# Performance work log

Measured on AMD Instinct MI355X. Metric: run time of the kernel, lower is better.

Reference implementation:

```python
import jax, jax.numpy as jnp
import numpy as np

N_HEAD, D_MODEL, D_K, D_V = 16, 1024, 64, 64
B, L = 8, 1024
LN_EPS = 1e-5
NEG_INF = -1e9


def setup_inputs() -> dict:
    key = jax.random.key(0)
    ks = jax.random.split(key, 12)
    s = 0.02
    return {
        "q": jax.random.normal(ks[0], (B, L, D_MODEL), jnp.float32),
        "k": jax.random.normal(ks[1], (B, L, D_MODEL), jnp.float32),
        "v": jax.random.normal(ks[2], (B, L, D_MODEL), jnp.float32),
        "mask": jnp.zeros((B, L, L), dtype=bool),
        "wq": jax.random.normal(ks[3], (D_MODEL, N_HEAD * D_K), jnp.float32) * s,
        "bq": jnp.zeros((N_HEAD * D_K,), jnp.float32),
        "wk": jax.random.normal(ks[4], (D_MODEL, N_HEAD * D_K), jnp.float32) * s,
        "bk": jnp.zeros((N_HEAD * D_K,), jnp.float32),
        "wv": jax.random.normal(ks[5], (D_MODEL, N_HEAD * D_V), jnp.float32) * s,
        "bv": jnp.zeros((N_HEAD * D_V,), jnp.float32),
        "wo": jax.random.normal(ks[6], (N_HEAD * D_V, D_MODEL), jnp.float32) * s,
        "bo": jnp.zeros((D_MODEL,), jnp.float32),
        "gamma": jnp.ones((D_MODEL,), jnp.float32),
        "beta": jnp.zeros((D_MODEL,), jnp.float32),
    }


def reference(q, k, v, mask, wq, bq, wk, bk, wv, bv, wo, bo, gamma, beta):
    b, lq, _ = q.shape
    lk = k.shape[1]
    residual = q
    # separate Q/K/V projections, split heads: [b, len, h, d]
    qh = (q @ wq + bq).reshape(b, lq, N_HEAD, D_K)
    kh = (k @ wk + bk).reshape(b, lk, N_HEAD, D_K)
    vh = (v @ wv + bv).reshape(b, lk, N_HEAD, D_V)
    # scaled dot-product attention (temperature = sqrt(d_k))
    scores = jnp.einsum("bqhd,bkhd->bhqk", qh, kh) / jnp.sqrt(jnp.float32(D_K))
    scores = jnp.where(mask[:, None, :, :], NEG_INF, scores)
    attn = jax.nn.softmax(scores, axis=-1)  # [b, h, lq, lk]
    ctx = jnp.einsum("bhqk,bkhd->bqhd", attn, vh).reshape(b, lq, N_HEAD * D_V)
    # out-proj (dropout is identity in eval) + residual + LayerNorm
    out = ctx @ wo + bo + residual
    mu = out.mean(-1, keepdims=True)
    var = out.var(-1, keepdims=True)
    out = (out - mu) * jax.lax.rsqrt(var + LN_EPS) * gamma + beta
    # match original attn layout: [n_head*b, lq, lk]
    attn_flat = attn.transpose(1, 0, 2, 3).reshape(N_HEAD * b, lq, lk)
    return out, attn_flat
```

## Files before the change

### kernel.cpp

```cpp
#include <hip/hip_runtime.h>
#include <stdint.h>

static constexpr int BATCH  = 8;
static constexpr int SEQ    = 1024;
static constexpr int DMODEL = 1024;
static constexpr int NHEAD  = 16;

typedef __attribute__((ext_vector_type(8))) short sh8;
typedef __attribute__((ext_vector_type(4))) float fl4;

__device__ __forceinline__ uint16_t f2bf(float f) {
    union { float f; uint32_t u; } a; a.f = f;
    uint32_t r = a.u + 0x7FFFu + ((a.u >> 16) & 1u);
    return (uint16_t)(r >> 16);
}

__device__ __forceinline__ float b2f(uint16_t u) {
    union { uint32_t u; float f; } a; a.u = ((uint32_t)u) << 16; return a.f;
}

__device__ __forceinline__ uint32_t cvtpk(float lo, float hi) {
    uint32_t r;
    asm("v_cvt_pk_bf16_f32 %0, %1, %2" : "=v"(r) : "v"(lo), "v"(hi));
    return r;
}

__device__ __forceinline__ sh8 pack_bf8(fl4 x0, fl4 x1) {
    union { uint32_t w[4]; sh8 v; } pk;
    pk.w[0] = cvtpk(x0[0], x0[1]); pk.w[1] = cvtpk(x0[2], x0[3]);
    pk.w[2] = cvtpk(x1[0], x1[1]); pk.w[3] = cvtpk(x1[2], x1[3]);
    return pk.v;
}

__device__ __forceinline__ fl4 mfma16(sh8 a, sh8 b, fl4 c) {
    return __builtin_amdgcn_mfma_f32_16x16x32_bf16(a, b, c, 0, 0, 0);
}

__device__ __forceinline__ void gload16(const void* g, void* l) {
    __builtin_amdgcn_global_load_lds(
        (const __attribute__((address_space(1))) void*)g,
        (__attribute__((address_space(3))) void*)l, 16, 0, 0);
}

__global__ __launch_bounds__(256) void prep_kernel(const float* __restrict__ wq, const float* __restrict__ wk,
                                                   const float* __restrict__ wv, const float* __restrict__ wo,
                                                   uint16_t* __restrict__ tq, uint16_t* __restrict__ tk,
                                                   uint16_t* __restrict__ tv, uint16_t* __restrict__ to) {
    __shared__ uint16_t T[64][72];
    const int z = blockIdx.z;
    const int tid = threadIdx.x;
    const float* w = (z == 0) ? wq : (z == 1) ? wk : (z == 2) ? wv : wo;
    uint16_t* wT = (z == 0) ? tq : (z == 1) ? tk : (z == 2) ? tv : to;
    const float ws = (z == 0) ? 0.125f : 1.f;
    const int n0 = blockIdx.x * 64, k0 = blockIdx.y * 64;
    #pragma unroll
    for (int it = 0; it < 4; ++it) {
        int g = it * 256 + tid;
        int r = g >> 4, c = (g & 15) * 4;
        fl4 x = *(const fl4*)(w + (size_t)(k0 + r) * DMODEL + n0 + c);
        T[r][c + 0] = f2bf(x[0] * ws); T[r][c + 1] = f2bf(x[1] * ws);
        T[r][c + 2] = f2bf(x[2] * ws); T[r][c + 3] = f2bf(x[3] * ws);
    }
    __syncthreads();
    #pragma unroll
    for (int it = 0; it < 4; ++it) {
        int g = it * 256 + tid;
        int r = g >> 4, c = (g & 15) * 4;
        ushort4 o;
        o.x = T[c + 0][r]; o.y = T[c + 1][r]; o.z = T[c + 2][r]; o.w = T[c + 3][r];
        *(ushort4*)(wT + (size_t)(n0 + r) * DMODEL + k0 + c) = o;
    }
}

__global__ __launch_bounds__(256)
void gemm_proj(const float* __restrict__ q, const float* __restrict__ k, const float* __restrict__ v,
               const uint16_t* __restrict__ B0, const uint16_t* __restrict__ B1, const uint16_t* __restrict__ B2,
               const float* __restrict__ b0, const float* __restrict__ b1, const float* __restrict__ b2,
               uint16_t* __restrict__ qh, uint16_t* __restrict__ kh, uint16_t* __restrict__ vT) {
    __shared__ uint16_t lds[128 * 128];
    uint16_t* Alds = lds;
    uint16_t* Blds = lds + 128 * 64;
    const int z = blockIdx.z;
    const float* Af    = (z == 0) ? q : (z == 1) ? k : v;
    const uint16_t* Bt = (z == 0) ? B0 : (z == 1) ? B1 : B2;
    const float* bias  = (z == 0) ? b0 : (z == 1) ? b1 : b2;
    const float bs     = (z == 0) ? 0.125f : 1.f;
    const int m0 = blockIdx.x * 128, n0 = blockIdx.y * 128;
    const int tid = threadIdx.x, lane = tid & 63, wid = tid >> 6;
    const int wr = (wid >> 1) * 64, wc = (wid & 1) * 64;
    const int fr = lane & 15, fk = (lane >> 4) * 8, frow4 = (lane >> 4) * 4;

    fl4 acc[4][4];
    #pragma unroll
    for (int i = 0; i < 4; ++i)
        #pragma unroll
        for (int j = 0; j < 4; ++j) acc[i][j] = (fl4){0.f, 0.f, 0.f, 0.f};

    fl4 pa0[4], pa1[4];
    #pragma unroll
    for (int it = 0; it < 4; ++it) {
        const int g = it * 256 + tid;
        const int r = g >> 3, c = (g & 7) << 3;
        const float* p = Af + (size_t)(m0 + r) * DMODEL + c;
        pa0[it] = *(const fl4*)p; pa1[it] = *(const fl4*)(p + 4);
    }

    for (int kt = 0; kt < 16; ++kt) {
        const int kb = kt * 64;
        #pragma unroll
        for (int it = 0; it < 4; ++it) {
            const int g = it * 256 + tid;
            const int r = g >> 3, c = (g & 7) << 3;
            *(sh8*)&Alds[r * 64 + c] = pack_bf8(pa0[it], pa1[it]);
            const int lofs = __builtin_amdgcn_readfirstlane((it * 256 + wid * 64) * 16);
            gload16(Bt + (size_t)(n0 + r) * DMODEL + kb + c, (char*)Blds + lofs);
        }
        __syncthreads();
        if (kt < 15) {
            #pragma unroll
            for (int it = 0; it < 4; ++it) {
                const int g = it * 256 + tid;
                const int r = g >> 3, c = (g & 7) << 3;
                const float* p = Af + (size_t)(m0 + r) * DMODEL + kb + 64 + c;
                pa0[it] = *(const fl4*)p; pa1[it] = *(const fl4*)(p + 4);
            }
        }
        #pragma unroll
        for (int ks = 0; ks < 2; ++ks) {
            sh8 a[4], bb[4];
            #pragma unroll
            for (int mi = 0; mi < 4; ++mi) a[mi] = *(const sh8*)&Alds[(wr + mi * 16 + fr) * 64 + ks * 32 + fk];
            #pragma unroll
            for (int ni = 0; ni < 4; ++ni) bb[ni] = *(const sh8*)&Blds[(wc + ni * 16 + fr) * 64 + ks * 32 + fk];
            #pragma unroll
            for (int mi = 0; mi < 4; ++mi)
                #pragma unroll
                for (int ni = 0; ni < 4; ++ni) acc[mi][ni] = mfma16(a[mi], bb[ni], acc[mi][ni]);
        }
        __syncthreads();
    }

    if (z < 2) {
        #pragma unroll
        for (int mi = 0; mi < 4; ++mi) {
            #pragma unroll
            for (int ni = 0; ni < 4; ++ni) {
                const int col = wc + ni * 16 + fr;
                const float bv = bias[n0 + col] * bs;
                #pragma unroll
                for (int i = 0; i < 4; ++i) {
                    const int row = wr + mi * 16 + frow4 + i;
                    lds[row * 128 + ((((col >> 3) ^ (row & 7)) << 3) | (col & 7))] = f2bf(acc[mi][ni][i] + bv);
                }
            }
        }
        __syncthreads();
        uint16_t* Cv = (z == 0) ? qh : kh;
        #pragma unroll
        for (int it = 0; it < 8; ++it) {
            const int ch = it * 256 + tid;
            const int row = ch >> 4, cc = ch & 15;
            sh8 vv = *(sh8*)&lds[row * 128 + ((cc ^ (row & 7)) << 3)];
            *(sh8*)(Cv + (size_t)(m0 + row) * DMODEL + n0 + cc * 8) = vv;
        }
    } else {
        #pragma unroll
        for (int mi = 0; mi < 4; ++mi) {
            #pragma unroll
            for (int ni = 0; ni < 4; ++ni) {
                const int col = wc + ni * 16 + fr;
                const float bv = bias[n0 + col];
                #pragma unroll
                for (int i = 0; i < 4; ++i) {
                    const int row = wr + mi * 16 + frow4 + i;
                    lds[col * 128 + ((((row >> 3) ^ (col & 7)) << 3) | (row & 7))] = f2bf(acc[mi][ni][i] + bv);
                }
            }
        }
        __syncthreads();
        const int b = m0 >> 10, l0 = m0 & 1023;
        #pragma unroll
        for (int it = 0; it < 8; ++it) {
            const int ch = it * 256 + tid;
            const int col = ch >> 4, rc = ch & 15;
            sh8 vv = *(sh8*)&lds[col * 128 + ((rc ^ (col & 7)) << 3)];
            *(sh8*)(vT + (size_t)(b * 1024 + n0 + col) * SEQ + l0 + rc * 8) = vv;
        }
    }
}

__global__ __launch_bounds__(256)
void gemm_out(const uint16_t* __restrict__ Ab, const uint16_t* __restrict__ Bt,
              const float* __restrict__ bias, const float* __restrict__ resid,
              float* __restrict__ Cv) {
    __shared__ uint16_t lds[128 * 128];
    uint16_t* Alds = lds;
    uint16_t* Blds = lds + 128 * 64;
    const int m0 = blockIdx.x * 128, n0 = blockIdx.y * 128;
    const int tid = threadIdx.x, lane = tid & 63, wid = tid >> 6;
    const int wr = (wid >> 1) * 64, wc = (wid & 1) * 64;
    const int fr = lane & 15, fk = (lane >> 4) * 8, frow4 = (lane >> 4) * 4;

    fl4 acc[4][4];
    #pragma unroll
    for (int i = 0; i < 4; ++i)
        #pragma unroll
        for (int j = 0; j < 4; ++j) acc[i][j] = (fl4){0.f, 0.f, 0.f, 0.f};

    for (int kt = 0; kt < 16; ++kt) {
        const int kb = kt * 64;
        #pragma unroll
        for (int it = 0; it < 4; ++it) {
            const int g = it * 256 + tid;
            const int r = g >> 3, c = (g & 7) << 3;
            const int lofs = __builtin_amdgcn_readfirstlane((it * 256 + wid * 64) * 16);
            gload16(Ab + (size_t)(m0 + r) * DMODEL + kb + c, (char*)Alds + lofs);
            gload16(Bt + (size_t)(n0 + r) * DMODEL + kb + c, (char*)Blds + lofs);
        }
        __syncthreads();
        #pragma unroll
        for (int ks = 0; ks < 2; ++ks) {
            sh8 a[4], bb[4];
            #pragma unroll
            for (int mi = 0; mi < 4; ++mi) a[mi] = *(const sh8*)&Alds[(wr + mi * 16 + fr) * 64 + ks * 32 + fk];
            #pragma unroll
            for (int ni = 0; ni < 4; ++ni) bb[ni] = *(const sh8*)&Blds[(wc + ni * 16 + fr) * 64 + ks * 32 + fk];
            #pragma unroll
            for (int mi = 0; mi < 4; ++mi)
                #pragma unroll
                for (int ni = 0; ni < 4; ++ni) acc[mi][ni] = mfma16(a[mi], bb[ni], acc[mi][ni]);
        }
        __syncthreads();
    }

    float* flds = (float*)lds;
    #pragma unroll
    for (int h2 = 0; h2 < 2; ++h2) {
        if (h2) __syncthreads();
        if (wc == h2 * 64) {
            #pragma unroll
            for (int ni = 0; ni < 4; ++ni) {
                const int col = wc + ni * 16 + fr;
                const int ch = col - h2 * 64;
                const float bv = bias[n0 + col];
                #pragma unroll
                for (int mi = 0; mi < 4; ++mi) {
                    #pragma unroll
                    for (int i = 0; i < 4; ++i) {
                        const int row = wr + mi * 16 + frow4 + i;
                        float val = acc[mi][ni][i] + bv;
                        val += resid[(size_t)(m0 + row) * DMODEL + n0 + col];
                        flds[row * 64 + ((((ch >> 2) ^ (row & 7)) << 2) | (ch & 3))] = val;
                    }
                }
            }
        }
        __syncthreads();
        #pragma unroll
        for (int it = 0; it < 8; ++it) {
            const int ck = it * 256 + tid;
            const int row = ck >> 4, cc = ck & 15;
            fl4 vv = *(fl4*)&flds[row * 64 + ((cc ^ (row & 7)) << 2)];
            *(fl4*)(Cv + (size_t)(m0 + row) * DMODEL + n0 + h2 * 64 + cc * 4) = vv;
        }
    }
}

__global__ __launch_bounds__(256)
void attn_kernel(const uint16_t* __restrict__ qh, const uint16_t* __restrict__ kh,
                 const uint16_t* __restrict__ vT, const uint8_t* __restrict__ mask,
                 float* __restrict__ attn, uint16_t* __restrict__ ctx) {
    __shared__ uint16_t S[16 * 1024];
    __shared__ float rinv[16];
    const int b = blockIdx.x, h = blockIdx.y, q0 = blockIdx.z * 16;
    const int tid = threadIdx.x, lane = tid & 63, wid = tid >> 6;
    const int fr = lane & 15, fk = (lane >> 4) * 8, frow4 = (lane >> 4) * 4;

    sh8 Aq[2];
    #pragma unroll
    for (int ks = 0; ks < 2; ++ks)
        Aq[ks] = *(const sh8*)(qh + (size_t)(b * SEQ + q0 + fr) * DMODEL + h * 64 + ks * 32 + fk);

    for (int t8 = 0; t8 < 8; ++t8) {
        const int kv0 = (t8 * 4 + wid) * 32;
        sh8 Bk[2][2];
        #pragma unroll
        for (int ni = 0; ni < 2; ++ni)
            #pragma unroll
            for (int ks = 0; ks < 2; ++ks)
                Bk[ni][ks] = *(const sh8*)(kh + (size_t)(b * SEQ + kv0 + ni * 16 + fr) * DMODEL + h * 64 + ks * 32 + fk);
        fl4 sa[2];
        #pragma unroll
        for (int ni = 0; ni < 2; ++ni) sa[ni] = (fl4){0.f, 0.f, 0.f, 0.f};
        #pragma unroll
        for (int ni = 0; ni < 2; ++ni)
            #pragma unroll
            for (int ks = 0; ks < 2; ++ks) sa[ni] = mfma16(Aq[ks], Bk[ni][ks], sa[ni]);
        #pragma unroll
        for (int ni = 0; ni < 2; ++ni)
            #pragma unroll
            for (int i = 0; i < 4; ++i) {
                const int row = frow4 + i, col = kv0 + ni * 16 + fr;
                S[row * 1024 + ((((col >> 3) ^ (row & 15)) << 3) | (col & 7))] = f2bf(sa[ni][i]);
            }
    }
    __syncthreads();

    {
        const int r = tid >> 4, j = tid & 15;
        const int rbase = r * 1024;
        const uint8_t* mbase = mask + (size_t)(b * SEQ + q0 + r) * SEQ;
        sh8 x[8];
        uint2 mw[8];
        #pragma unroll
        for (int c4 = 0; c4 < 8; ++c4) {
            const int cc = c4 * 16 + j;
            x[c4] = *(sh8*)&S[rbase + ((cc ^ r) << 3)];
            mw[c4] = *(const uint2*)(mbase + cc * 8);
        }
        uint32_t anym = 0;
        #pragma unroll
        for (int c4 = 0; c4 < 8; ++c4) anym |= (mw[c4].x | mw[c4].y);
        float mx = -1e30f;
        if (anym == 0) {
            #pragma unroll
            for (int c4 = 0; c4 < 8; ++c4)
                #pragma unroll
                for (int t = 0; t < 8; ++t) mx = fmaxf(mx, b2f((uint16_t)x[c4][t]));
        } else {
            #pragma unroll
            for (int c4 = 0; c4 < 8; ++c4) {
                float f[8];
                #pragma unroll
                for (int t = 0; t < 4; ++t)
                    f[t] = ((mw[c4].x >> (t * 8)) & 0xFF) ? -1e9f : b2f((uint16_t)x[c4][t]);
                #pragma unroll
                for (int t = 0; t < 4; ++t)
                    f[4 + t] = ((mw[c4].y >> (t * 8)) & 0xFF) ? -1e9f : b2f((uint16_t)x[c4][4 + t]);
                union { uint32_t w[4]; sh8 v; } pk;
                pk.w[0] = cvtpk(f[0], f[1]); pk.w[1] = cvtpk(f[2], f[3]);
                pk.w[2] = cvtpk(f[4], f[5]); pk.w[3] = cvtpk(f[6], f[7]);
                x[c4] = pk.v;
                #pragma unroll
                for (int t = 0; t < 8; ++t) mx = fmaxf(mx, f[t]);
            }
        }
        #pragma unroll
        for (int d = 1; d < 16; d <<= 1) mx = fmaxf(mx, __shfl_xor(mx, d));
        float sum = 0.f;
        #pragma unroll
        for (int c4 = 0; c4 < 8; ++c4) {
            const int cc = c4 * 16 + j;
            float e[8];
            #pragma unroll
            for (int t = 0; t < 8; ++t) e[t] = __expf(b2f((uint16_t)x[c4][t]) - mx);
            union { uint32_t w[4]; sh8 v; } pk;
            pk.w[0] = cvtpk(e[0], e[1]); pk.w[1] = cvtpk(e[2], e[3]);
            pk.w[2] = cvtpk(e[4], e[5]); pk.w[3] = cvtpk(e[6], e[7]);
            *(sh8*)&S[rbase + ((cc ^ r) << 3)] = pk.v;
            sum += e[0] + e[1] + e[2] + e[3] + e[4] + e[5] + e[6] + e[7];
        }
        #pragma unroll
        for (int d = 1; d < 16; d <<= 1) sum += __shfl_xor(sum, d);
        if (j == 0) rinv[r] = 1.f / sum;
    }
    __syncthreads();

    {
        float* ab = attn + ((size_t)((h * BATCH + b) * SEQ + q0)) * SEQ;
        #pragma unroll
        for (int it = 0; it < 16; ++it) {
            const int ch = it * 256 + tid;
            const int row = ch >> 8, oc = ch & 255;
            const int cc = oc >> 1, half = oc & 1;
            const ushort4 p = *(const ushort4*)&S[row * 1024 + ((cc ^ row) << 3) + half * 4];
            const float ri = rinv[row];
            fl4 o;
            o[0] = b2f(p.x) * ri; o[1] = b2f(p.y) * ri;
            o[2] = b2f(p.z) * ri; o[3] = b2f(p.w) * ri;
            __builtin_nontemporal_store(o, (fl4*)(ab + (size_t)ch * 4));
        }
    }

    fl4 acc0 = (fl4){0.f, 0.f, 0.f, 0.f}, acc1 = (fl4){0.f, 0.f, 0.f, 0.f};
    const uint16_t* vbase = vT + (size_t)((b * NHEAD + h) * 64 + wid * 16) * SEQ;
    #pragma unroll 4
    for (int ks2 = 0; ks2 < 32; ++ks2) {
        const int kv = ks2 * 32;
        sh8 Ap = *(const sh8*)&S[fr * 1024 + ((((kv + fk) >> 3) ^ fr) << 3)];
        sh8 Bv = *(const sh8*)(vbase + (size_t)fr * SEQ + kv + fk);
        if (ks2 & 1) acc1 = mfma16(Ap, Bv, acc1);
        else         acc0 = mfma16(Ap, Bv, acc0);
    }
    __syncthreads();

    {
        uint16_t* Sc = S;
        #pragma unroll
        for (int i = 0; i < 4; ++i) {
            const int qr = frow4 + i;
            Sc[qr * 64 + wid * 16 + fr] = f2bf((acc0[i] + acc1[i]) * rinv[qr]);
        }
        __syncthreads();
        const int row = tid >> 4, c4 = (tid & 15) * 4;
        ushort4 vv = *(ushort4*)&Sc[row * 64 + c4];
        *(ushort4*)(ctx + (size_t)(b * SEQ + q0 + row) * DMODEL + h * 64 + c4) = vv;
    }
}

__global__ __launch_bounds__(256)
void ln_kernel(const float* __restrict__ raw, const float* __restrict__ gamma,
               const float* __restrict__ beta, float* __restrict__ out) {
    const int row = blockIdx.x;
    const int tid = threadIdx.x;
    const float* x = raw + (size_t)row * DMODEL;
    fl4 xv = *(const fl4*)(x + tid * 4);
    float s  = xv[0] + xv[1] + xv[2] + xv[3];
    float ss = xv[0] * xv[0] + xv[1] * xv[1] + xv[2] * xv[2] + xv[3] * xv[3];
    #pragma unroll
    for (int d = 1; d < 64; d <<= 1) { s += __shfl_xor(s, d); ss += __shfl_xor(ss, d); }
    __shared__ float sb[4], ssb[4];
    if ((tid & 63) == 0) { sb[tid >> 6] = s; ssb[tid >> 6] = ss; }
    __syncthreads();
    s  = sb[0] + sb[1] + sb[2] + sb[3];
    ss = ssb[0] + ssb[1] + ssb[2] + ssb[3];
    const float mu  = s * (1.f / 1024.f);
    const float var = ss * (1.f / 1024.f) - mu * mu;
    const float rstd = rsqrtf(var + 1e-5f);
    fl4 g  = *(const fl4*)(gamma + tid * 4);
    fl4 be = *(const fl4*)(beta + tid * 4);
    fl4 o;
    #pragma unroll
    for (int j = 0; j < 4; ++j) o[j] = (xv[j] - mu) * rstd * g[j] + be[j];
    *(fl4*)(out + (size_t)row * DMODEL + tid * 4) = o;
}

extern "C" void kernel_launch(void* const* d_in, const int* in_sizes, int n_in,
                              void* d_out, int out_size, void* d_ws, size_t ws_size,
                              hipStream_t stream) {
    (void)in_sizes; (void)n_in; (void)out_size; (void)ws_size;
    const float* q     = (const float*)d_in[0];
    const float* k     = (const float*)d_in[1];
    const float* v     = (const float*)d_in[2];
    const uint8_t* mask = (const uint8_t*)d_in[3];
    const float* wq = (const float*)d_in[4];
    const float* bq = (const float*)d_in[5];
    const float* wk = (const float*)d_in[6];
    const float* bk = (const float*)d_in[7];
    const float* wv = (const float*)d_in[8];
    const float* bv = (const float*)d_in[9];
    const float* wo = (const float*)d_in[10];
    const float* bo = (const float*)d_in[11];
    const float* gamma = (const float*)d_in[12];
    const float* beta  = (const float*)d_in[13];

    float* out  = (float*)d_out;
    float* attn = out + (size_t)BATCH * SEQ * DMODEL;

    char* ws = (char*)d_ws;
    uint16_t* qh   = (uint16_t*)(ws);
    uint16_t* kh   = (uint16_t*)(ws + ((size_t)16 << 20));
    uint16_t* vT   = (uint16_t*)(ws + ((size_t)32 << 20));
    uint16_t* ctx  = (uint16_t*)(ws + ((size_t)48 << 20));
    uint16_t* wqT  = (uint16_t*)(ws + ((size_t)64 << 20));
    uint16_t* wkT  = (uint16_t*)(ws + ((size_t)66 << 20));
    uint16_t* wvT  = (uint16_t*)(ws + ((size_t)68 << 20));
    uint16_t* woT  = (uint16_t*)(ws + ((size_t)70 << 20));

    dim3 tb(256);
    prep_kernel<<<dim3(16, 16, 4), tb, 0, stream>>>(wq, wk, wv, wo, wqT, wkT, wvT, woT);

    gemm_proj<<<dim3(64, 8, 3), tb, 0, stream>>>(q, k, v, wqT, wkT, wvT,
                                                 bq, bk, bv, qh, kh, vT);

    attn_kernel<<<dim3(BATCH, NHEAD, 64), tb, 0, stream>>>(qh, kh, vT, mask, attn, ctx);

    gemm_out<<<dim3(64, 8), tb, 0, stream>>>(ctx, woT, bo, q, out);

    ln_kernel<<<BATCH * SEQ, tb, 0, stream>>>(out, gamma, beta, out);
}
```

Before: 412.2 us.

## Double-buffer LDS tiles in projection and output GEMMs to overlap loads

Both GEMM kernels move from a single LDS tile to ping-pong buffers: B (and A for the output GEMM) for step k+1 is prefetched asynchronously while the MFMAs for step k run. In the output GEMM this also removes one barrier per K iteration. The intent is to hide global-to-LDS latency behind compute. The cost is more LDS per block (48KB and 64KB), which could reduce occupancy.

After: 425.9 us. +3.3%, slower.

```diff
diff --git a/kernel.cpp b/kernel.cpp
--- a/kernel.cpp
+++ b/kernel.cpp
@@ -77,9 +77,8 @@
                const uint16_t* __restrict__ B0, const uint16_t* __restrict__ B1, const uint16_t* __restrict__ B2,
                const float* __restrict__ b0, const float* __restrict__ b1, const float* __restrict__ b2,
                uint16_t* __restrict__ qh, uint16_t* __restrict__ kh, uint16_t* __restrict__ vT) {
-    __shared__ uint16_t lds[128 * 128];
-    uint16_t* Alds = lds;
-    uint16_t* Blds = lds + 128 * 64;
+    __shared__ uint16_t Alds[128 * 64];
+    __shared__ uint16_t Bbuf[2 * 128 * 64];
     const int z = blockIdx.z;
     const float* Af    = (z == 0) ? q : (z == 1) ? k : v;
     const uint16_t* Bt = (z == 0) ? B0 : (z == 1) ? B1 : B2;
@@ -103,35 +102,41 @@
         const int r = g >> 3, c = (g & 7) << 3;
         const float* p = Af + (size_t)(m0 + r) * DMODEL + c;
         pa0[it] = *(const fl4*)p; pa1[it] = *(const fl4*)(p + 4);
+        *(sh8*)&Alds[r * 64 + c] = pack_bf8(pa0[it], pa1[it]);
+        const int lofs = __builtin_amdgcn_readfirstlane((it * 256 + wid * 64) * 16);
+        gload16(Bt + (size_t)(n0 + r) * DMODEL + c, (char*)Bbuf + lofs);
     }
 
     for (int kt = 0; kt < 16; ++kt) {
-        const int kb = kt * 64;
-        #pragma unroll
-        for (int it = 0; it < 4; ++it) {
-            const int g = it * 256 + tid;
-            const int r = g >> 3, c = (g & 7) << 3;
-            *(sh8*)&Alds[r * 64 + c] = pack_bf8(pa0[it], pa1[it]);
-            const int lofs = __builtin_amdgcn_readfirstlane((it * 256 + wid * 64) * 16);
-            gload16(Bt + (size_t)(n0 + r) * DMODEL + kb + c, (char*)Blds + lofs);
-        }
-        __syncthreads();
-        if (kt < 15) {
+        if (kt > 0) {
             #pragma unroll
             for (int it = 0; it < 4; ++it) {
                 const int g = it * 256 + tid;
                 const int r = g >> 3, c = (g & 7) << 3;
-                const float* p = Af + (size_t)(m0 + r) * DMODEL + kb + 64 + c;
+                *(sh8*)&Alds[r * 64 + c] = pack_bf8(pa0[it], pa1[it]);
+            }
+        }
+        __syncthreads();
+        if (kt < 15) {
+            const int boff = ((kt + 1) & 1) * 128 * 64 * 2;
+            #pragma unroll
+            for (int it = 0; it < 4; ++it) {
+                const int g = it * 256 + tid;
+                const int r = g >> 3, c = (g & 7) << 3;
+                const int lofs = __builtin_amdgcn_readfirstlane((it * 256 + wid * 64) * 16);
+                gload16(Bt + (size_t)(n0 + r) * DMODEL + (kt + 1) * 64 + c, (char*)Bbuf + boff + lofs);
+                const float* p = Af + (size_t)(m0 + r) * DMODEL + (kt + 1) * 64 + c;
                 pa0[it] = *(const fl4*)p; pa1[it] = *(const fl4*)(p + 4);
             }
         }
+        const uint16_t* Bl = Bbuf + (kt & 1) * 128 * 64;
         #pragma unroll
         for (int ks = 0; ks < 2; ++ks) {
             sh8 a[4], bb[4];
             #pragma unroll
             for (int mi = 0; mi < 4; ++mi) a[mi] = *(const sh8*)&Alds[(wr + mi * 16 + fr) * 64 + ks * 32 + fk];
             #pragma unroll
-            for (int ni = 0; ni < 4; ++ni) bb[ni] = *(const sh8*)&Blds[(wc + ni * 16 + fr) * 64 + ks * 32 + fk];
+            for (int ni = 0; ni < 4; ++ni) bb[ni] = *(const sh8*)&Bl[(wc + ni * 16 + fr) * 64 + ks * 32 + fk];
             #pragma unroll
             for (int mi = 0; mi < 4; ++mi)
                 #pragma unroll
@@ -140,6 +145,7 @@
         __syncthreads();
     }
 
+    uint16_t* lds = Bbuf;
     if (z < 2) {
         #pragma unroll
         for (int mi = 0; mi < 4; ++mi) {
@@ -193,9 +199,8 @@
 void gemm_out(const uint16_t* __restrict__ Ab, const uint16_t* __restrict__ Bt,
               const float* __restrict__ bias, const float* __restrict__ resid,
               float* __restrict__ Cv) {
-    __shared__ uint16_t lds[128 * 128];
-    uint16_t* Alds = lds;
-    uint16_t* Blds = lds + 128 * 64;
+    __shared__ uint16_t Ab2[2 * 128 * 64];
+    __shared__ uint16_t Bb2[2 * 128 * 64];
     const int m0 = blockIdx.x * 128, n0 = blockIdx.y * 128;
     const int tid = threadIdx.x, lane = tid & 63, wid = tid >> 6;
     const int wr = (wid >> 1) * 64, wc = (wid & 1) * 64;
@@ -207,33 +212,46 @@
         #pragma unroll
         for (int j = 0; j < 4; ++j) acc[i][j] = (fl4){0.f, 0.f, 0.f, 0.f};
 
+    #pragma unroll
+    for (int it = 0; it < 4; ++it) {
+        const int g = it * 256 + tid;
+        const int r = g >> 3, c = (g & 7) << 3;
+        const int lofs = __builtin_amdgcn_readfirstlane((it * 256 + wid * 64) * 16);
+        gload16(Ab + (size_t)(m0 + r) * DMODEL + c, (char*)Ab2 + lofs);
+        gload16(Bt + (size_t)(n0 + r) * DMODEL + c, (char*)Bb2 + lofs);
+    }
+
     for (int kt = 0; kt < 16; ++kt) {
-        const int kb = kt * 64;
-        #pragma unroll
-        for (int it = 0; it < 4; ++it) {
-            const int g = it * 256 + tid;
-            const int r = g >> 3, c = (g & 7) << 3;
-            const int lofs = __builtin_amdgcn_readfirstlane((it * 256 + wid * 64) * 16);
-            gload16(Ab + (size_t)(m0 + r) * DMODEL + kb + c, (char*)Alds + lofs);
-            gload16(Bt + (size_t)(n0 + r) * DMODEL + kb + c, (char*)Blds + lofs);
-        }
-        __syncthreads();
+        __syncthreads();
+        if (kt < 15) {
+            const int boff = ((kt + 1) & 1) * 128 * 64 * 2;
+            #pragma unroll
+            for (int it = 0; it < 4; ++it) {
+                const int g = it * 256 + tid;
+                const int r = g >> 3, c = (g & 7) << 3;
+                const int lofs = __builtin_amdgcn_readfirstlane((it * 256 + wid * 64) * 16);
+                gload16(Ab + (size_t)(m0 + r) * DMODEL + (kt + 1) * 64 + c, (char*)Ab2 + boff + lofs);
+                gload16(Bt + (size_t)(n0 + r) * DMODEL + (kt + 1) * 64 + c, (char*)Bb2 + boff + lofs);
+            }
+        }
+        const uint16_t* Al = Ab2 + (kt & 1) * 128 * 64;
+        const uint16_t* Bl = Bb2 + (kt & 1) * 128 * 64;
         #pragma unroll
         for (int ks = 0; ks < 2; ++ks) {
             sh8 a[4], bb[4];
             #pragma unroll
-            for (int mi = 0; mi < 4; ++mi) a[mi] = *(const sh8*)&Alds[(wr + mi * 16 + fr) * 64 + ks * 32 + fk];
-            #pragma unroll
-            for (int ni = 0; ni < 4; ++ni) bb[ni] = *(const sh8*)&Blds[(wc + ni * 16 + fr) * 64 + ks * 32 + fk];
+            for (int mi = 0; mi < 4; ++mi) a[mi] = *(const sh8*)&Al[(wr + mi * 16 + fr) * 64 + ks * 32 + fk];
+            #pragma unroll
+            for (int ni = 0; ni < 4; ++ni) bb[ni] = *(const sh8*)&Bl[(wc + ni * 16 + fr) * 64 + ks * 32 + fk];
             #pragma unroll
             for (int mi = 0; mi < 4; ++mi)
                 #pragma unroll
                 for (int ni = 0; ni < 4; ++ni) acc[mi][ni] = mfma16(a[mi], bb[ni], acc[mi][ni]);
         }
-        __syncthreads();
-    }
-
-    float* flds = (float*)lds;
+    }
+    __syncthreads();
+
+    float* flds = (float*)Ab2;
     #pragma unroll
     for (int h2 = 0; h2 < 2; ++h2) {
         if (h2) __syncthreads();
```
